# Optimization experiments

Measured on AMD Instinct MI355X. Metric: run time of the kernel, lower is better.

The kernel has to match this reference:

```python
import jax, jax.numpy as jnp
import numpy as np

N = 80000   # nodes
E = 320000  # directed edges
B = 3200    # graphs (25 nodes each)
D = 256     # emb_dim
L = 5       # num_layer
SIZES = [121, 8, 12, 15, 10, 9, 7, 3, 3]          # atom-feature vocab sizes
ESIZES = [25, 6, 2]                               # bond-feature vocab sizes
OFFS = np.concatenate([[0], np.cumsum(SIZES)[:-1]])  # offsets into fused node table
BN_EPS = 1e-5


def setup_inputs() -> dict:
    key = jax.random.key(0)
    ks = jax.random.split(key, 32)
    # int node features, per-column vocab bound
    x = jnp.stack([jax.random.randint(ks[i], (N,), 0, SIZES[i]) for i in range(9)], axis=1)
    edge_index = jax.random.randint(ks[9], (2, E), 0, N)
    edge_attr = jnp.stack([jax.random.randint(ks[10 + j], (E,), 0, ESIZES[j]) for j in range(3)], axis=1)
    batch = jnp.arange(N) // (N // B)  # sorted graph ids, 25 nodes per graph
    s = 0.1
    node_emb = jax.random.normal(ks[13], (int(sum(SIZES)), D)) * s  # fused 9 tables
    edge_emb1 = jax.random.normal(ks[14], (L, 25, D)) * s
    edge_emb2 = jax.random.normal(ks[15], (L, 6, D)) * s
    edge_emb3 = jax.random.normal(ks[16], (L, 2, D)) * s
    w = 0.05
    W1 = jax.random.normal(ks[17], (L, D, 2 * D)) * w
    b1 = jnp.zeros((L, 2 * D))
    W2 = jax.random.normal(ks[18], (L, 2 * D, D)) * w
    b2 = jnp.zeros((L, D))
    bn_g = jnp.ones((L, D))
    bn_b = jnp.zeros((L, D))
    H = D // 2
    HW1 = jax.random.normal(ks[19], (D, H)) * w
    Hb1 = jnp.zeros((H,))
    HW2 = jax.random.normal(ks[20], (H, H)) * w
    Hb2 = jnp.zeros((H,))
    HW3 = jax.random.normal(ks[21], (H, 2)) * w
    Hb3 = jnp.zeros((2,))
    return {"x": x, "edge_index": edge_index, "edge_attr": edge_attr, "batch": batch,
            "node_emb": node_emb, "edge_emb1": edge_emb1, "edge_emb2": edge_emb2,
            "edge_emb3": edge_emb3, "W1": W1, "b1": b1, "W2": W2, "b2": b2,
            "bn_g": bn_g, "bn_b": bn_b, "HW1": HW1, "Hb1": Hb1, "HW2": HW2,
            "Hb2": Hb2, "HW3": HW3, "Hb3": Hb3}


def _gnn_graphpred(x, edge_index, edge_attr, batch, node_emb, edge_emb1, edge_emb2,
                   edge_emb3, W1, b1, W2, b2, bn_g, bn_b, HW1, Hb1, HW2, Hb2, HW3, Hb3):
    n = x.shape[0]
    offs = jnp.asarray(OFFS, dtype=x.dtype)
    # sum of 9 atom embeddings == one gather into fused table
    h = node_emb[x + offs[None, :]].sum(axis=1)            # [N, D]
    # add self loops; self-loop edge_attr = [22, 0, 0]
    loop = jnp.arange(n, dtype=edge_index.dtype)
    src = jnp.concatenate([edge_index[0], loop])
    dst = jnp.concatenate([edge_index[1], loop])
    ea0 = jnp.concatenate([edge_attr[:, 0], jnp.full((n,), 22, edge_attr.dtype)])
    ea1 = jnp.concatenate([edge_attr[:, 1], jnp.zeros((n,), edge_attr.dtype)])
    ea2 = jnp.concatenate([edge_attr[:, 2], jnp.zeros((n,), edge_attr.dtype)])
    nl = W1.shape[0]
    relu_flag = jnp.arange(nl) < (nl - 1)   # ReLU on all but last layer (JK='last')

    def layer(hc, p):
        e1, e2, e3, w1, bb1, w2, bb2, g, b, flag = p
        eemb = e1[ea0] + e2[ea1] + e3[ea2]                 # [E+N, D]
        msg = hc[src] + eemb                                # gather + add
        aggr = jax.ops.segment_sum(msg, dst, num_segments=n)  # scatter-sum
        h2 = jax.nn.relu(aggr @ w1 + bb1) @ w2 + bb2        # GIN MLP
        mean = h2.mean(axis=0)
        var = h2.var(axis=0)                                # BatchNorm (batch stats)
        h2 = (h2 - mean) * jax.lax.rsqrt(var + BN_EPS) * g + b
        h2 = jnp.where(flag, jax.nn.relu(h2), h2)
        return h2, None

    h, _ = jax.lax.scan(layer, h, (edge_emb1, edge_emb2, edge_emb3, W1, b1, W2, b2,
                                   bn_g, bn_b, relu_flag))
    # super_node_rep: last node of each graph (batch is sorted)
    last_idx = jax.ops.segment_max(jnp.arange(n), batch, num_segments=B)
    super_rep = h[last_idx]                                 # [B, D]
    z = jax.nn.elu(super_rep @ HW1 + Hb1)
    z = jax.nn.elu(z @ HW2 + Hb2)
    return z @ HW3 + Hb3                                    # [B, 2]


def reference(x, edge_index, edge_attr, batch, node_emb, edge_emb1, edge_emb2,
              edge_emb3, W1, b1, W2, b2, bn_g, bn_b, HW1, Hb1, HW2, Hb2, HW3, Hb3):
    return _gnn_graphpred(x, edge_index, edge_attr, batch, node_emb, edge_emb1,
                          edge_emb2, edge_emb3, W1, b1, W2, b2, bn_g, bn_b,
                          HW1, Hb1, HW2, Hb2, HW3, Hb3)
```

## Files before the change

### kernel.cpp

```cpp
#include <hip/hip_runtime.h>
#include <hip/hip_bf16.h>

#define NN 80000
#define EE 320000
#define ET 400000
#define BB 3200
#define LL 5
#define NBLK 313

typedef __attribute__((ext_vector_type(8))) short bf16x8;
typedef __attribute__((ext_vector_type(4))) float f32x4;

__device__ __forceinline__ float bf2f(unsigned short u) {
    unsigned int v = ((unsigned int)u) << 16;
    return __builtin_bit_cast(float, v);
}
__device__ __forceinline__ unsigned short f2bf(float f) {
    return __builtin_bit_cast(unsigned short, __float2bfloat16(f));
}


__global__ void k_deg(const int* ei, int* deg) {
    int e = blockIdx.x * 256 + threadIdx.x;
    if (e >= ET) return;
    int d = (e < EE) ? ei[EE + e] : (e - EE);
    atomicAdd(&deg[d], 1);
}

__global__ void k_scan1(const int* deg, int* blksum) {
    __shared__ int sh[256];
    int t = threadIdx.x, b = blockIdx.x;
    int i = b * 256 + t;
    int v = (i < NN) ? deg[i] : 0;
    sh[t] = v; __syncthreads();
    for (int off = 128; off > 0; off >>= 1) {
        if (t < off) sh[t] += sh[t + off];
        __syncthreads();
    }
    if (t == 0) blksum[b] = sh[0];
}

__global__ __launch_bounds__(512) void k_scan2(const int* blksum, int* blkoff) {
    __shared__ int sh[512];
    int t = threadIdx.x;
    int v = (t < NBLK) ? blksum[t] : 0;
    sh[t] = v; __syncthreads();
    for (int off = 1; off < 512; off <<= 1) {
        int x = (t >= off) ? sh[t - off] : 0;
        __syncthreads();
        sh[t] += x;
        __syncthreads();
    }
    if (t < NBLK) blkoff[t] = sh[t] - v;
}

__global__ void k_scan3(const int* deg, const int* blkoff, int* row_start, int* cursor) {
    __shared__ int sh[256];
    int t = threadIdx.x, b = blockIdx.x;
    int i = b * 256 + t;
    int v = (i < NN) ? deg[i] : 0;
    sh[t] = v; __syncthreads();
    for (int off = 1; off < 256; off <<= 1) {
        int x = (t >= off) ? sh[t - off] : 0;
        __syncthreads();
        sh[t] += x;
        __syncthreads();
    }
    int exc = sh[t] - v + blkoff[b];
    if (i < NN) { row_start[i] = exc; cursor[i] = exc; }
    if (i == NN - 1) row_start[NN] = exc + v;
}

__global__ void k_fill(const int* ei, const int* ea, int* cursor, int* eid, int* combo) {
    int e = blockIdx.x * 256 + threadIdx.x;
    if (e >= ET) return;
    int d = (e < EE) ? ei[EE + e] : (e - EE);
    int p = atomicAdd(&cursor[d], 1);
    eid[p] = e;
    int c;
    if (e < EE) c = ea[e * 3 + 0] * 12 + ea[e * 3 + 1] * 2 + ea[e * 3 + 2];
    else        c = 22 * 12;
    combo[e] = c;
}

__global__ void k_sortbkt(const int* row_start, int* eid) {
    int v = blockIdx.x * 256 + threadIdx.x;
    if (v >= NN) return;
    int s0 = row_start[v], s1 = row_start[v + 1];
    for (int i = s0 + 1; i < s1; i++) {
        int key = eid[i];
        int j = i - 1;
        while (j >= s0 && eid[j] > key) { eid[j + 1] = eid[j]; j--; }
        eid[j + 1] = key;
    }
}

__global__ void k_remap(const int* eid, const int* combo, const int* ei_src,
                        int* csrc, int* ccomb) {
    int p = blockIdx.x * 256 + threadIdx.x;
    if (p >= ET) return;
    int e = eid[p];
    csrc[p]  = (e < EE) ? ei_src[e] : (e - EE);
    ccomb[p] = combo[e];
}

__global__ void k_ecomb(const float* e1, const float* e2, const float* e3, float* ec) {
    int l = blockIdx.x / 300, c = blockIdx.x % 300, d = threadIdx.x;
    int a0 = c / 12, a1 = (c / 2) % 6, a2 = c & 1;
    ec[(size_t)(l * 300 + c) * 256 + d] =
        e1[(size_t)(l * 25 + a0) * 256 + d] +
        e2[(size_t)(l * 6 + a1) * 256 + d] +
        e3[(size_t)(l * 2 + a2) * 256 + d];
}

__global__ void k_w1t(const float* W, __hip_bfloat16* Wt) {
    int i = blockIdx.x * 256 + threadIdx.x;
    if (i >= LL * 512 * 256) return;
    int l = i / (512 * 256); int r = i % (512 * 256); int n = r / 256; int k = r % 256;
    Wt[i] = __float2bfloat16(W[(size_t)(l * 256 + k) * 512 + n]);
}
__global__ void k_w2t(const float* W, __hip_bfloat16* Wt) {
    int i = blockIdx.x * 256 + threadIdx.x;
    if (i >= LL * 256 * 512) return;
    int l = i / (256 * 512); int r = i % (256 * 512); int n = r / 512; int k = r % 512;
    Wt[i] = __float2bfloat16(W[(size_t)(l * 512 + k) * 256 + n]);
}

__global__ void k_nodeemb(const int* x, const float* emb, __hip_bfloat16* h) {
    const int offs[9] = {0, 121, 129, 141, 156, 166, 175, 182, 185};
    int i = blockIdx.x; int d = threadIdx.x;
    float acc = 0.f;
#pragma unroll
    for (int c = 0; c < 9; c++) {
        int idx = x[i * 9 + c] + offs[c];
        acc += emb[(size_t)idx * 256 + d];
    }
    h[(size_t)i * 256 + d] = __float2bfloat16(acc);
}


__global__ __launch_bounds__(256) void k_aggr(const __hip_bfloat16* h, const float* ecomb_l,
        const int* row_start, const int* csrc, const int* ccomb,
        __hip_bfloat16* aggrB) {
    int v = blockIdx.x * 4 + (threadIdx.x >> 6);
    if (v >= NN) return;
    int lane = threadIdx.x & 63;
    int s0 = row_start[v], s1 = row_start[v + 1];
    const unsigned short* hp = (const unsigned short*)h;
    float a0 = 0.f, a1 = 0.f, a2 = 0.f, a3 = 0.f;
    for (int p = s0; p < s1; p++) {
        int s = csrc[p];
        int c = ccomb[p];
        ushort4 hv = *(const ushort4*)(hp + (size_t)s * 256 + lane * 4);
        f32x4 ev = *(const f32x4*)(ecomb_l + (size_t)c * 256 + lane * 4);
        a0 += bf2f(hv.x) + ev.x;
        a1 += bf2f(hv.y) + ev.y;
        a2 += bf2f(hv.z) + ev.z;
        a3 += bf2f(hv.w) + ev.w;
    }
    ushort4 o;
    o.x = f2bf(a0); o.y = f2bf(a1);
    o.z = f2bf(a2); o.w = f2bf(a3);
    *(ushort4*)((unsigned short*)aggrB + (size_t)v * 256 + lane * 4) = o;
}

template<int K, bool RELU, bool OUTBF, bool STATS>
__global__ __launch_bounds__(256) void k_gemm(const __hip_bfloat16* A, const __hip_bfloat16* Wt,
                                              const float* bias, void* out, int Nn,
                                              float* psum, float* psq) {
    __shared__ short lA[128 * 32];
    __shared__ short lB[128 * 32];
    __shared__ float redS[4][64], redQ[4][64];
    int tid = threadIdx.x;
    int wave = tid >> 6, lane = tid & 63;
    int mBase = blockIdx.x * 128;
    int nBase = blockIdx.y * 128;
    int wr = (wave >> 1) * 64;
    int wc = (wave & 1) * 64;
    int lr = lane & 15, lk = lane >> 4;
    const short* Ap = (const short*)A + (size_t)mBase * K;
    const short* Bp = (const short*)Wt + (size_t)nBase * K;
    int srow = (lane >> 2);
    int scol = (lane & 3) * 8;
    f32x4 acc[4][4] = {};

    for (int k0 = 0; k0 < K; k0 += 32) {
#pragma unroll
        for (int i = 0; i < 2; i++) {
            int chunk = wave * 2 + i;
            int row = chunk * 16 + srow;
            __builtin_amdgcn_global_load_lds(
                (const __attribute__((address_space(1))) unsigned int*)(Ap + (size_t)row * K + k0 + scol),
                (__attribute__((address_space(3))) unsigned int*)(&lA[chunk * 512]), 16, 0, 0);
            __builtin_amdgcn_global_load_lds(
                (const __attribute__((address_space(1))) unsigned int*)(Bp + (size_t)row * K + k0 + scol),
                (__attribute__((address_space(3))) unsigned int*)(&lB[chunk * 512]), 16, 0, 0);
        }
        __syncthreads();
        bf16x8 a[4], b[4];
#pragma unroll
        for (int m = 0; m < 4; m++)
            a[m] = *(const bf16x8*)(&lA[(wr + m * 16 + lr) * 32 + lk * 8]);
#pragma unroll
        for (int n = 0; n < 4; n++)
            b[n] = *(const bf16x8*)(&lB[(wc + n * 16 + lr) * 32 + lk * 8]);
#pragma unroll
        for (int m = 0; m < 4; m++)
#pragma unroll
            for (int n = 0; n < 4; n++)
                acc[m][n] = __builtin_amdgcn_mfma_f32_16x16x32_bf16(a[m], b[n], acc[m][n], 0, 0, 0);
        __syncthreads();
    }

    float colS[4] = {0.f, 0.f, 0.f, 0.f}, colQ[4] = {0.f, 0.f, 0.f, 0.f};
#pragma unroll
    for (int m = 0; m < 4; m++)
#pragma unroll
        for (int n = 0; n < 4; n++) {
            int cdx = nBase + wc + n * 16 + lr;
            float bi = bias[cdx];
#pragma unroll
            for (int j = 0; j < 4; j++) {
                int r = mBase + wr + m * 16 + lk * 4 + j;
                float v = acc[m][n][j] + bi;
                if (RELU) v = fmaxf(v, 0.f);
                if (OUTBF) ((__hip_bfloat16*)out)[(size_t)r * Nn + cdx] = __float2bfloat16(v);
                else       ((float*)out)[(size_t)r * Nn + cdx] = v;
                if (STATS) { colS[n] += v; colQ[n] += v * v; }
            }
        }

    if (STATS) {
#pragma unroll
        for (int n = 0; n < 4; n++) {
            for (int off = 16; off < 64; off <<= 1) {
                colS[n] += __shfl_xor(colS[n], off);
                colQ[n] += __shfl_xor(colQ[n], off);
            }
        }
        if (lk == 0) {
#pragma unroll
            for (int n = 0; n < 4; n++) {
                redS[wave][n * 16 + lr] = colS[n];
                redQ[wave][n * 16 + lr] = colQ[n];
            }
        }
        __syncthreads();
        if (tid < 128) {
            int c = tid;
            int w0 = (c < 64) ? 0 : 1;
            int cc = c & 63;
            float S = redS[w0][cc] + redS[w0 + 2][cc];
            float Q = redQ[w0][cc] + redQ[w0 + 2][cc];
            psum[(size_t)(nBase + c) * 625 + blockIdx.x] = S;
            psq [(size_t)(nBase + c) * 625 + blockIdx.x] = Q;
        }
    }
}

__global__ __launch_bounds__(256) void k_bn2(const float* psum, const float* psq,
                                             const float* g, const float* bta, float* stat) {
    __shared__ float s1[256], s2[256];
    int d = blockIdx.x; int t = threadIdx.x;
    float a = 0.f, b = 0.f;
    for (int rb = t; rb < 625; rb += 256) {
        a += psum[(size_t)d * 625 + rb];
        b += psq [(size_t)d * 625 + rb];
    }
    s1[t] = a; s2[t] = b; __syncthreads();
    for (int off = 128; off > 0; off >>= 1) {
        if (t < off) { s1[t] += s1[t + off]; s2[t] += s2[t + off]; }
        __syncthreads();
    }
    if (t == 0) {
        float mean = s1[0] / NN;
        float var = s2[0] / NN - mean * mean;
        float sc = rsqrtf(var + 1e-5f) * g[d];
        stat[d] = sc;
        stat[256 + d] = bta[d] - mean * sc;
    }
}

__global__ void k_bnapply(const float* h2, const float* stat, __hip_bfloat16* h, int relu) {
    int i = (blockIdx.x * 256 + threadIdx.x) * 4;
    int d = i & 255;
    f32x4 v = *(const f32x4*)(h2 + i);
    f32x4 sc = *(const f32x4*)(stat + d);
    f32x4 sh = *(const f32x4*)(stat + 256 + d);
    float r0 = v.x * sc.x + sh.x;
    float r1 = v.y * sc.y + sh.y;
    float r2 = v.z * sc.z + sh.z;
    float r3 = v.w * sc.w + sh.w;
    if (relu) {
        r0 = fmaxf(r0, 0.f); r1 = fmaxf(r1, 0.f);
        r2 = fmaxf(r2, 0.f); r3 = fmaxf(r3, 0.f);
    }
    ushort4 o;
    o.x = f2bf(r0); o.y = f2bf(r1); o.z = f2bf(r2); o.w = f2bf(r3);
    *(ushort4*)((unsigned short*)h + i) = o;
}


__global__ __launch_bounds__(128) void k_head(const __hip_bfloat16* h,
        const float* HW1, const float* Hb1, const float* HW2, const float* Hb2,
        const float* HW3, const float* Hb3, float* out) {
    __shared__ float row[256], z1[128], z2[128];
    int g = blockIdx.x; int t = threadIdx.x;
    size_t node = (size_t)g * 25 + 24;
    row[t]       = __bfloat162float(h[node * 256 + t]);
    row[t + 128] = __bfloat162float(h[node * 256 + t + 128]);
    __syncthreads();
    float acc = Hb1[t];
    for (int k = 0; k < 256; k++) acc += row[k] * HW1[k * 128 + t];
    z1[t] = acc > 0.f ? acc : expm1f(acc);
    __syncthreads();
    acc = Hb2[t];
    for (int k = 0; k < 128; k++) acc += z1[k] * HW2[k * 128 + t];
    z2[t] = acc > 0.f ? acc : expm1f(acc);
    __syncthreads();
    if (t < 2) {
        acc = Hb3[t];
        for (int k = 0; k < 128; k++) acc += z2[k] * HW3[k * 2 + t];
        out[g * 2 + t] = acc;
    }
}


extern "C" void kernel_launch(void* const* d_in, const int* in_sizes, int n_in,
                              void* d_out, int out_size, void* d_ws, size_t ws_size,
                              hipStream_t stream) {
    const int* x          = (const int*)d_in[0];
    const int* edge_index = (const int*)d_in[1];
    const int* edge_attr  = (const int*)d_in[2];
    const float* node_emb = (const float*)d_in[4];
    const float* ee1 = (const float*)d_in[5];
    const float* ee2 = (const float*)d_in[6];
    const float* ee3 = (const float*)d_in[7];
    const float* W1  = (const float*)d_in[8];
    const float* b1  = (const float*)d_in[9];
    const float* W2  = (const float*)d_in[10];
    const float* b2  = (const float*)d_in[11];
    const float* bng = (const float*)d_in[12];
    const float* bnb = (const float*)d_in[13];
    const float* HW1 = (const float*)d_in[14];
    const float* Hb1 = (const float*)d_in[15];
    const float* HW2 = (const float*)d_in[16];
    const float* Hb2 = (const float*)d_in[17];
    const float* HW3 = (const float*)d_in[18];
    const float* Hb3 = (const float*)d_in[19];
    float* out = (float*)d_out;

    char* ws = (char*)d_ws;
    size_t off = 0;
    auto alloc = [&](size_t bytes) -> char* {
        off = (off + 255) & ~(size_t)255;
        char* p = ws + off;
        off += bytes;
        return p;
    };
    int* deg       = (int*)alloc((size_t)NN * 4);
    int* cursor    = (int*)alloc((size_t)NN * 4);
    int* row_start = (int*)alloc((size_t)(NN + 1) * 4);
    int* blksum    = (int*)alloc((size_t)(NBLK + 1) * 4);
    int* blkoff    = (int*)alloc((size_t)(NBLK + 1) * 4);
    int* eid       = (int*)alloc((size_t)ET * 4);
    int* combo     = (int*)alloc((size_t)ET * 4);
    int* csrc      = (int*)alloc((size_t)ET * 4);
    int* ccomb     = (int*)alloc((size_t)ET * 4);
    float* ecomb   = (float*)alloc((size_t)LL * 300 * 256 * 4);
    __hip_bfloat16* W1t = (__hip_bfloat16*)alloc((size_t)LL * 512 * 256 * 2);
    __hip_bfloat16* W2t = (__hip_bfloat16*)alloc((size_t)LL * 256 * 512 * 2);
    __hip_bfloat16* h    = (__hip_bfloat16*)alloc((size_t)NN * 256 * 2);
    __hip_bfloat16* aggrB = (__hip_bfloat16*)alloc((size_t)NN * 256 * 2);
    __hip_bfloat16* act  = (__hip_bfloat16*)alloc((size_t)NN * 512 * 2);
    float* h2     = (float*)alloc((size_t)NN * 256 * 4);
    float* psum   = (float*)alloc((size_t)256 * 625 * 4);
    float* psq    = (float*)alloc((size_t)256 * 625 * 4);
    float* bnstat = (float*)alloc((size_t)512 * 4);

    hipMemsetAsync(deg, 0, (size_t)NN * 4, stream);
    k_deg<<<(ET + 255) / 256, 256, 0, stream>>>(edge_index, deg);
    k_scan1<<<NBLK, 256, 0, stream>>>(deg, blksum);
    k_scan2<<<1, 512, 0, stream>>>(blksum, blkoff);
    k_scan3<<<NBLK, 256, 0, stream>>>(deg, blkoff, row_start, cursor);
    k_fill<<<(ET + 255) / 256, 256, 0, stream>>>(edge_index, edge_attr, cursor, eid, combo);
    k_sortbkt<<<(NN + 255) / 256, 256, 0, stream>>>(row_start, eid);
    k_remap<<<(ET + 255) / 256, 256, 0, stream>>>(eid, combo, edge_index, csrc, ccomb);
    k_ecomb<<<LL * 300, 256, 0, stream>>>(ee1, ee2, ee3, ecomb);
    k_w1t<<<(LL * 512 * 256 + 255) / 256, 256, 0, stream>>>(W1, W1t);
    k_w2t<<<(LL * 256 * 512 + 255) / 256, 256, 0, stream>>>(W2, W2t);
    k_nodeemb<<<NN, 256, 0, stream>>>(x, node_emb, h);

    for (int l = 0; l < LL; l++) {
        k_aggr<<<(NN + 3) / 4, 256, 0, stream>>>(h, ecomb + (size_t)l * 300 * 256, row_start,
                                                 csrc, ccomb, aggrB);
        k_gemm<256, true, true, false><<<dim3(625, 4), 256, 0, stream>>>(
            aggrB, W1t + (size_t)l * 512 * 256, b1 + l * 512, act, 512, nullptr, nullptr);
        k_gemm<512, false, false, true><<<dim3(625, 2), 256, 0, stream>>>(
            act, W2t + (size_t)l * 256 * 512, b2 + l * 256, h2, 256, psum, psq);
        k_bn2<<<256, 256, 0, stream>>>(psum, psq, bng + l * 256, bnb + l * 256, bnstat);
        k_bnapply<<<NN * 256 / (256 * 4), 256, 0, stream>>>(h2, bnstat, h, (l < LL - 1) ? 1 : 0);
    }

    k_head<<<BB, 128, 0, stream>>>(h, HW1, Hb1, HW2, Hb2, HW3, Hb3, out);
}
```

Before: 1.037 ms.

## Double-buffer GEMM LDS with swizzle, widen aggr loads, fuse final BN into head

The GEMM now prefetches the next K-tile into a second LDS buffer while computing the current one, and XOR-swizzles LDS columns to reduce bank conflicts. The aggregation kernel processes two nodes per wave using 16-byte bf16 loads per lane. The final layer's BN-apply pass is skipped: the head applies the BN scale and shift directly to the last node of each graph. In exchange, LDS use doubles and the kernels become more complex, with some risk of a sync hazard around the double buffer.

```diff
diff --git a/kernel.cpp b/kernel.cpp
--- a/kernel.cpp
+++ b/kernel.cpp
@@ -9,6 +9,7 @@
 #define NBLK 313
 
 typedef __attribute__((ext_vector_type(8))) short bf16x8;
+typedef __attribute__((ext_vector_type(8))) unsigned short u16x8;
 typedef __attribute__((ext_vector_type(4))) float f32x4;
 
 __device__ __forceinline__ float bf2f(unsigned short u) {
@@ -142,34 +143,40 @@
 __global__ __launch_bounds__(256) void k_aggr(const __hip_bfloat16* h, const float* ecomb_l,
         const int* row_start, const int* csrc, const int* ccomb,
         __hip_bfloat16* aggrB) {
-    int v = blockIdx.x * 4 + (threadIdx.x >> 6);
-    if (v >= NN) return;
+    int wid = threadIdx.x >> 6;
     int lane = threadIdx.x & 63;
+    int v = blockIdx.x * 8 + wid * 2 + (lane >> 5);
+    int sl = lane & 31;
     int s0 = row_start[v], s1 = row_start[v + 1];
     const unsigned short* hp = (const unsigned short*)h;
-    float a0 = 0.f, a1 = 0.f, a2 = 0.f, a3 = 0.f;
+    float acc[8] = {0.f, 0.f, 0.f, 0.f, 0.f, 0.f, 0.f, 0.f};
     for (int p = s0; p < s1; p++) {
         int s = csrc[p];
         int c = ccomb[p];
-        ushort4 hv = *(const ushort4*)(hp + (size_t)s * 256 + lane * 4);
-        f32x4 ev = *(const f32x4*)(ecomb_l + (size_t)c * 256 + lane * 4);
-        a0 += bf2f(hv.x) + ev.x;
-        a1 += bf2f(hv.y) + ev.y;
-        a2 += bf2f(hv.z) + ev.z;
-        a3 += bf2f(hv.w) + ev.w;
-    }
-    ushort4 o;
-    o.x = f2bf(a0); o.y = f2bf(a1);
-    o.z = f2bf(a2); o.w = f2bf(a3);
-    *(ushort4*)((unsigned short*)aggrB + (size_t)v * 256 + lane * 4) = o;
+        u16x8 hv = *(const u16x8*)(hp + (size_t)s * 256 + sl * 8);
+        f32x4 e0 = *(const f32x4*)(ecomb_l + (size_t)c * 256 + sl * 8);
+        f32x4 e1 = *(const f32x4*)(ecomb_l + (size_t)c * 256 + sl * 8 + 4);
+        acc[0] += bf2f(hv[0]) + e0.x;
+        acc[1] += bf2f(hv[1]) + e0.y;
+        acc[2] += bf2f(hv[2]) + e0.z;
+        acc[3] += bf2f(hv[3]) + e0.w;
+        acc[4] += bf2f(hv[4]) + e1.x;
+        acc[5] += bf2f(hv[5]) + e1.y;
+        acc[6] += bf2f(hv[6]) + e1.z;
+        acc[7] += bf2f(hv[7]) + e1.w;
+    }
+    u16x8 o;
+#pragma unroll
+    for (int j = 0; j < 8; j++) o[j] = f2bf(acc[j]);
+    *(u16x8*)((unsigned short*)aggrB + (size_t)v * 256 + sl * 8) = o;
 }
 
 template<int K, bool RELU, bool OUTBF, bool STATS>
 __global__ __launch_bounds__(256) void k_gemm(const __hip_bfloat16* A, const __hip_bfloat16* Wt,
                                               const float* bias, void* out, int Nn,
                                               float* psum, float* psq) {
-    __shared__ short lA[128 * 32];
-    __shared__ short lB[128 * 32];
+    __shared__ short lA[2][128 * 32];
+    __shared__ short lB[2][128 * 32];
     __shared__ float redS[4][64], redQ[4][64];
     int tid = threadIdx.x;
     int wave = tid >> 6, lane = tid & 63;
@@ -180,30 +187,43 @@
     int lr = lane & 15, lk = lane >> 4;
     const short* Ap = (const short*)A + (size_t)mBase * K;
     const short* Bp = (const short*)Wt + (size_t)nBase * K;
-    int srow = (lane >> 2);
-    int scol = (lane & 3) * 8;
+    int srow = lane >> 2;
+    int sslot = lane & 3;
     f32x4 acc[4][4] = {};
-
-    for (int k0 = 0; k0 < K; k0 += 32) {
+    constexpr int NT = K / 32;
+
+    auto stage = [&](int buf, int k0) {
 #pragma unroll
         for (int i = 0; i < 2; i++) {
             int chunk = wave * 2 + i;
-            int row = chunk * 16 + srow;
+            int r = chunk * 16 + srow;
+            int scol = (sslot ^ ((r ^ (r >> 2)) & 3)) * 8;
             __builtin_amdgcn_global_load_lds(
-                (const __attribute__((address_space(1))) unsigned int*)(Ap + (size_t)row * K + k0 + scol),
-                (__attribute__((address_space(3))) unsigned int*)(&lA[chunk * 512]), 16, 0, 0);
+                (const __attribute__((address_space(1))) unsigned int*)(Ap + (size_t)r * K + k0 + scol),
+                (__attribute__((address_space(3))) unsigned int*)(&lA[buf][chunk * 512]), 16, 0, 0);
             __builtin_amdgcn_global_load_lds(
-                (const __attribute__((address_space(1))) unsigned int*)(Bp + (size_t)row * K + k0 + scol),
-                (__attribute__((address_space(3))) unsigned int*)(&lB[chunk * 512]), 16, 0, 0);
-        }
-        __syncthreads();
+                (const __attribute__((address_space(1))) unsigned int*)(Bp + (size_t)r * K + k0 + scol),
+                (__attribute__((address_space(3))) unsigned int*)(&lB[buf][chunk * 512]), 16, 0, 0);
+        }
+    };
+
+    stage(0, 0);
+    __syncthreads();
+
+    for (int t = 0; t < NT; t++) {
+        int cur = t & 1;
+        if (t + 1 < NT) stage(cur ^ 1, (t + 1) * 32);
         bf16x8 a[4], b[4];
 #pragma unroll
-        for (int m = 0; m < 4; m++)
-            a[m] = *(const bf16x8*)(&lA[(wr + m * 16 + lr) * 32 + lk * 8]);
-#pragma unroll
-        for (int n = 0; n < 4; n++)
-            b[n] = *(const bf16x8*)(&lB[(wc + n * 16 + lr) * 32 + lk * 8]);
+        for (int m = 0; m < 4; m++) {
+            int r = wr + m * 16 + lr;
+            a[m] = *(const bf16x8*)(&lA[cur][r * 32 + ((lk ^ ((r ^ (r >> 2)) & 3)) << 3)]);
+        }
+#pragma unroll
+        for (int n = 0; n < 4; n++) {
+            int r = wc + n * 16 + lr;
+            b[n] = *(const bf16x8*)(&lB[cur][r * 32 + ((lk ^ ((r ^ (r >> 2)) & 3)) << 3)]);
+        }
 #pragma unroll
         for (int m = 0; m < 4; m++)
 #pragma unroll
@@ -300,15 +320,14 @@
     *(ushort4*)((unsigned short*)h + i) = o;
 }
 
-
-__global__ __launch_bounds__(128) void k_head(const __hip_bfloat16* h,
+__global__ __launch_bounds__(128) void k_head(const float* h2, const float* stat,
         const float* HW1, const float* Hb1, const float* HW2, const float* Hb2,
         const float* HW3, const float* Hb3, float* out) {
     __shared__ float row[256], z1[128], z2[128];
     int g = blockIdx.x; int t = threadIdx.x;
     size_t node = (size_t)g * 25 + 24;
-    row[t]       = __bfloat162float(h[node * 256 + t]);
-    row[t + 128] = __bfloat162float(h[node * 256 + t + 128]);
+    row[t]       = h2[node * 256 + t] * stat[t] + stat[256 + t];
+    row[t + 128] = h2[node * 256 + t + 128] * stat[t + 128] + stat[256 + t + 128];
     __syncthreads();
     float acc = Hb1[t];
     for (int k = 0; k < 256; k++) acc += row[k] * HW1[k * 128 + t];
@@ -392,15 +411,16 @@
     k_nodeemb<<<NN, 256, 0, stream>>>(x, node_emb, h);
 
     for (int l = 0; l < LL; l++) {
-        k_aggr<<<(NN + 3) / 4, 256, 0, stream>>>(h, ecomb + (size_t)l * 300 * 256, row_start,
-                                                 csrc, ccomb, aggrB);
+        k_aggr<<<NN / 8, 256, 0, stream>>>(h, ecomb + (size_t)l * 300 * 256, row_start,
+                                           csrc, ccomb, aggrB);
         k_gemm<256, true, true, false><<<dim3(625, 4), 256, 0, stream>>>(
             aggrB, W1t + (size_t)l * 512 * 256, b1 + l * 512, act, 512, nullptr, nullptr);
         k_gemm<512, false, false, true><<<dim3(625, 2), 256, 0, stream>>>(
             act, W2t + (size_t)l * 256 * 512, b2 + l * 256, h2, 256, psum, psq);
         k_bn2<<<256, 256, 0, stream>>>(psum, psq, bng + l * 256, bnb + l * 256, bnstat);
-        k_bnapply<<<NN * 256 / (256 * 4), 256, 0, stream>>>(h2, bnstat, h, (l < LL - 1) ? 1 : 0);
-    }
-
-    k_head<<<BB, 128, 0, stream>>>(h, HW1, Hb1, HW2, Hb2, HW3, Hb3, out);
-}
+        if (l < LL - 1)
+            k_bnapply<<<NN * 256 / (256 * 4), 256, 0, stream>>>(h2, bnstat, h, 1);
+    }
+
+    k_head<<<BB, 128, 0, stream>>>(h2, bnstat, HW1, Hb1, HW2, Hb2, HW3, Hb3, out);
+}
```

New measurement: 944.3 us. -8.9%, faster.
